# Kernel optimization log

Measured on AMD Instinct MI355X. Metric: run time of the kernel, lower is better.

Reference implementation:

```python
import jax, jax.numpy as jnp
import numpy as np

D, H, FF, E, K, B, S = 1024, 16, 4096, 8, 2, 2, 2048
EPS = 1e-5


def _layernorm(x, g, b):
    mu = x.mean(-1, keepdims=True)
    var = x.var(-1, keepdims=True)
    return (x - mu) * jax.lax.rsqrt(var + EPS) * g + b


def setup_inputs() -> dict:
    key = jax.random.key(0)
    ks = jax.random.split(key, 16)
    s = 0.02
    return {
        "x": jax.random.normal(ks[0], (B, S, D), dtype=jnp.float32),
        "in_proj_w": jax.random.normal(ks[1], (3 * D, D), dtype=jnp.float32) * s,
        "in_proj_b": jnp.zeros((3 * D,), jnp.float32),
        "out_proj_w": jax.random.normal(ks[2], (D, D), dtype=jnp.float32) * s,
        "out_proj_b": jnp.zeros((D,), jnp.float32),
        "ln1_g": jnp.ones((D,), jnp.float32),
        "ln1_b": jnp.zeros((D,), jnp.float32),
        "ln2_g": jnp.ones((D,), jnp.float32),
        "ln2_b": jnp.zeros((D,), jnp.float32),
        "gate_w": jax.random.normal(ks[3], (E, D), dtype=jnp.float32) * s,
        "gate_b": jnp.zeros((E,), jnp.float32),
        "w1": jax.random.normal(ks[4], (E, FF, D), dtype=jnp.float32) * s,
        "b1": jnp.zeros((E, FF), jnp.float32),
        "w2": jax.random.normal(ks[5], (E, D, FF), dtype=jnp.float32) * s,
        "b2": jnp.zeros((E, D), jnp.float32),
    }


def reference(x, in_proj_w, in_proj_b, out_proj_w, out_proj_b,
              ln1_g, ln1_b, ln2_g, ln2_b,
              gate_w, gate_b, w1, b1, w2, b2):
    b, s, d = x.shape
    hd = d // H
    # --- self-attention (pre-LN), dropout = identity (eval) ---
    normed = _layernorm(x, ln1_g, ln1_b)
    qkv = normed @ in_proj_w.T + in_proj_b            # [b,s,3d]
    q, k, v = jnp.split(qkv, 3, axis=-1)
    q = q.reshape(b, s, H, hd).transpose(0, 2, 1, 3)  # [b,h,s,hd]
    k = k.reshape(b, s, H, hd).transpose(0, 2, 1, 3)
    v = v.reshape(b, s, H, hd).transpose(0, 2, 1, 3)
    scores = jnp.einsum('bhqe,bhke->bhqk', q, k) / np.sqrt(hd)
    attn = jax.nn.softmax(scores, axis=-1)
    o = jnp.einsum('bhqk,bhke->bhqe', attn, v)
    o = o.transpose(0, 2, 1, 3).reshape(b, s, d)
    attn_out = o @ out_proj_w.T + out_proj_b
    x = x + attn_out
    present_kv = (normed, normed)
    # --- MoE FFN ---
    n2 = _layernorm(x, ln2_g, ln2_b)
    xf = n2.reshape(-1, d)                             # [T,d]
    T = xf.shape[0]
    logits = xf @ gate_w.T + gate_b                    # [T,E]
    probs = jax.nn.softmax(logits, axis=-1)
    top_v, top_i = jax.lax.top_k(probs, K)             # [T,K]
    top_v = top_v / top_v.sum(-1, keepdims=True)
    # combine weights per (token, expert); topk indices are unique per token
    cw = jnp.zeros((T, E), probs.dtype).at[jnp.arange(T)[:, None], top_i].add(top_v)
    # dense all-experts FFN (mathematically identical to masked gather/scatter)
    h = jnp.einsum('td,efd->etf', xf, w1) + b1[:, None, :]   # [E,T,FF]
    h = jax.nn.gelu(h, approximate=False)
    eo = jnp.einsum('etf,edf->etd', h, w2) + b2[:, None, :]  # [E,T,d]
    moe_out = jnp.einsum('te,etd->td', cw, eo)               # [T,d]
    out = x + moe_out.reshape(b, s, d)
    # --- load balance loss (Switch) ---
    top1 = jnp.argmax(probs, axis=-1)
    f = jnp.mean(jax.nn.one_hot(top1, E, dtype=probs.dtype), axis=0)
    P = probs.mean(axis=0)
    load_loss = 0.01 * E * jnp.sum(f * P)
    return out, load_loss, probs.reshape(b, s, E), present_kv[0]
```

## Files before the change

kernel.cpp:

```cpp
#include <hip/hip_runtime.h>
#include <math.h>

#define D_ 1024
#define H_ 16
#define HD_ 64
#define FF_ 4096
#define E_ 8
#define B_ 2
#define S_ 2048
#define T_ 4096
#define MAXROWS 9216
#define MAXTILES 72

typedef unsigned short u16;
typedef __attribute__((ext_vector_type(4))) float f32x4;
typedef __attribute__((ext_vector_type(8))) __bf16 bf16x8;
typedef __attribute__((ext_vector_type(8))) _Float16 f16x8;
typedef __attribute__((ext_vector_type(4))) unsigned short u16x4;

__device__ __forceinline__ u16 f2bf(float f){
  union { float f; unsigned u; } v; v.f = f;
  unsigned r = v.u + 0x7fffu + ((v.u >> 16) & 1u);
  return (u16)(r >> 16);
}
__device__ __forceinline__ float bf2f(u16 h){
  union { unsigned u; float f; } v; v.u = ((unsigned)h) << 16;
  return v.f;
}
__device__ __forceinline__ void glds16(const void* g, void* l){
  __builtin_amdgcn_global_load_lds((const __attribute__((address_space(1))) void*)g,
                                   (__attribute__((address_space(3))) void*)l, 16, 0, 0);
}
__device__ __forceinline__ bf16x8 ld8(const u16* p){
  return *reinterpret_cast<const bf16x8*>(p);
}
__device__ __forceinline__ f16x8 ldH8(const _Float16* p){
  return *reinterpret_cast<const f16x8*>(p);
}
__device__ __forceinline__ f32x4 mfma16(bf16x8 a, bf16x8 b, f32x4 c){
  return __builtin_amdgcn_mfma_f32_16x16x32_bf16(a, b, c, 0, 0, 0);
}
__device__ __forceinline__ f32x4 mfmaH(f16x8 a, f16x8 b, f32x4 c){
  return __builtin_amdgcn_mfma_f32_16x16x32_f16(a, b, c, 0, 0, 0);
}
__device__ __forceinline__ unsigned pk16(float a, float b){
  auto pk = __builtin_amdgcn_cvt_pkrtz(a, b);
  return __builtin_bit_cast(unsigned, pk);
}

__global__ void __launch_bounds__(256) split_hl_f16_kernel(const float* __restrict__ in,
    _Float16* __restrict__ hi, _Float16* __restrict__ lo, int n4){
  int i = blockIdx.x*blockDim.x + threadIdx.x;
  if (i >= n4) return;
  float4 v = reinterpret_cast<const float4*>(in)[i];
  float vv[4] = {v.x, v.y, v.z, v.w};
  u16x4 h, l;
  #pragma unroll
  for (int j=0;j<4;j++){
    const _Float16 hh = (_Float16)vv[j];
    const _Float16 ll = (_Float16)(vv[j] - (float)hh);
    h[j] = __builtin_bit_cast(u16, hh);
    l[j] = __builtin_bit_cast(u16, ll);
  }
  reinterpret_cast<u16x4*>(hi)[i] = h;
  reinterpret_cast<u16x4*>(lo)[i] = l;
}

__global__ void __launch_bounds__(256) cvt_bf_kernel(const float* __restrict__ in, u16* __restrict__ out, int n4){
  int i = blockIdx.x*blockDim.x + threadIdx.x;
  if (i >= n4) return;
  float4 v = reinterpret_cast<const float4*>(in)[i];
  u16x4 o;
  o[0]=f2bf(v.x); o[1]=f2bf(v.y); o[2]=f2bf(v.z); o[3]=f2bf(v.w);
  reinterpret_cast<u16x4*>(out)[i] = o;
}

__global__ void __launch_bounds__(256) cvt_f16_kernel(const float* __restrict__ in, _Float16* __restrict__ out, int n4){
  int i = blockIdx.x*blockDim.x + threadIdx.x;
  if (i >= n4) return;
  float4 v = reinterpret_cast<const float4*>(in)[i];
  union { unsigned w[2]; u16x4 u; } o;
  o.w[0] = pk16(v.x, v.y);
  o.w[1] = pk16(v.z, v.w);
  reinterpret_cast<u16x4*>(out)[i] = o.u;
}

template<int OUTMODE, int GATE>
__global__ void __launch_bounds__(256) ln_kernel(const float* __restrict__ x, const float* __restrict__ g,
    const float* __restrict__ bta, float* __restrict__ outf, u16* __restrict__ nout,
    const float* __restrict__ gw, const float* __restrict__ gb,
    float* __restrict__ probs_out, int* __restrict__ top_i, float* __restrict__ cw_w)
{
  const int t = blockIdx.x, tid = threadIdx.x;
  __shared__ float rs[4], rq[4];
  __shared__ float sp[4][E_];
  const float4 v = reinterpret_cast<const float4*>(x + (size_t)t*D_)[tid];
  float s  = v.x+v.y+v.z+v.w;
  float s2 = v.x*v.x+v.y*v.y+v.z*v.z+v.w*v.w;
  #pragma unroll
  for (int o=32;o;o>>=1){ s += __shfl_xor(s,o); s2 += __shfl_xor(s2,o); }
  const int wid=tid>>6, lane=tid&63;
  if (lane==0){ rs[wid]=s; rq[wid]=s2; }
  __syncthreads();
  s  = rs[0]+rs[1]+rs[2]+rs[3];
  s2 = rq[0]+rq[1]+rq[2]+rq[3];
  const float mu  = s*(1.0f/D_);
  const float var = s2*(1.0f/D_) - mu*mu;
  const float inv = rsqrtf(var + 1e-5f);
  const float4 gv = reinterpret_cast<const float4*>(g)[tid];
  const float4 bv = reinterpret_cast<const float4*>(bta)[tid];
  float oo[4];
  oo[0] = (v.x-mu)*inv*gv.x + bv.x;
  oo[1] = (v.y-mu)*inv*gv.y + bv.y;
  oo[2] = (v.z-mu)*inv*gv.z + bv.z;
  oo[3] = (v.w-mu)*inv*gv.w + bv.w;
  const size_t base = (size_t)t*D_ + tid*4;
  if (outf){ outf[base]=oo[0]; outf[base+1]=oo[1]; outf[base+2]=oo[2]; outf[base+3]=oo[3]; }
  if (OUTMODE==1){
    union { unsigned w[2]; u16x4 u; } hv;
    hv.w[0] = pk16(oo[0], oo[1]);
    hv.w[1] = pk16(oo[2], oo[3]);
    reinterpret_cast<u16x4*>(nout)[base>>2] = hv.u;
  } else {
    u16x4 hv;
    hv[0]=f2bf(oo[0]); hv[1]=f2bf(oo[1]); hv[2]=f2bf(oo[2]); hv[3]=f2bf(oo[3]);
    reinterpret_cast<u16x4*>(nout)[base>>2] = hv;
  }
  if (GATE){
    float part[E_];
    #pragma unroll
    for (int e=0;e<E_;e++){
      const float4 wv = reinterpret_cast<const float4*>(gw + (size_t)e*D_)[tid];
      part[e] = oo[0]*wv.x + oo[1]*wv.y + oo[2]*wv.z + oo[3]*wv.w;
    }
    #pragma unroll
    for (int e=0;e<E_;e++){
      #pragma unroll
      for (int o=32;o;o>>=1) part[e] += __shfl_xor(part[e], o);
    }
    if (lane==0){
      #pragma unroll
      for (int e=0;e<E_;e++) sp[wid][e] = part[e];
    }
    __syncthreads();
    if (tid==0){
      float lg[E_], mx=-3e38f;
      #pragma unroll
      for (int e=0;e<E_;e++){
        lg[e] = sp[0][e]+sp[1][e]+sp[2][e]+sp[3][e] + gb[e];
        mx = fmaxf(mx, lg[e]);
      }
      float ex[E_], sm=0.f;
      #pragma unroll
      for (int e=0;e<E_;e++){ ex[e]=__expf(lg[e]-mx); sm+=ex[e]; }
      float p[E_];
      #pragma unroll
      for (int e=0;e<E_;e++){ p[e]=ex[e]/sm; probs_out[(size_t)t*E_+e]=p[e]; }
      int i0=0; float l0=lg[0];
      #pragma unroll
      for (int e=1;e<E_;e++) if (lg[e]>l0){ l0=lg[e]; i0=e; }
      int i1=-1; float l1=-3e38f;
      #pragma unroll
      for (int e=0;e<E_;e++) if (e!=i0 && lg[e]>l1){ l1=lg[e]; i1=e; }
      top_i[2*t]=i0; top_i[2*t+1]=i1;
      const float v0=p[i0], v1=p[i1];
      const float swt=v0+v1;
      cw_w[2*t]=v0/swt; cw_w[2*t+1]=v1/swt;
    }
  }
}

__global__ void __launch_bounds__(256) qkv_kernel(
    const _Float16* __restrict__ A, const _Float16* __restrict__ Bw,
    const float* __restrict__ bias,
    _Float16* __restrict__ qf, _Float16* __restrict__ kf, _Float16* __restrict__ vtf)
{
  __shared__ __align__(16) _Float16 Ash[2][128*32], Bsh[2][128*32];
  const int bid = blockIdx.x, nwg = gridDim.x;
  const int fid = (bid & 7)*(nwg>>3) + (bid>>3);
  const int nt = fid % 24, mt = fid / 24;
  const int tid=threadIdx.x, wid=tid>>6, lane=tid&63;
  const int wr=wid>>1, wc=wid&1;
  const int r16=lane&15, g4=lane>>4;
  const _Float16* Ag = A  + (size_t)mt*128*D_;
  const _Float16* Bg = Bw + (size_t)nt*128*D_;
  const int srow = wid*16 + (lane>>2);
  const int scol = (((lane&3) ^ ((lane>>3)&3)))*8;
  const int sl   = (g4 ^ ((r16>>1)&3))*8;
  f32x4 acc[4][4] = {};
#define QSTAGE(bi, k0) do { \
    _Pragma("unroll") \
    for (int p=0;p<2;p++){ \
      const int r  = p*64 + srow; \
      const int lo = (p*64 + wid*16)*32; \
      glds16(Ag + (size_t)r*D_ + (k0) + scol, &Ash[bi][lo]); \
      glds16(Bg + (size_t)r*D_ + (k0) + scol, &Bsh[bi][lo]); \
    } \
  } while(0)
  QSTAGE(0, 0);
  int cur = 0;
  for (int t=0; t<D_/32; ++t){
    if (t+1 < D_/32){
      QSTAGE(cur^1, (t+1)*32);
      asm volatile("s_waitcnt vmcnt(4)" ::: "memory");
    } else {
      asm volatile("s_waitcnt vmcnt(0)" ::: "memory");
    }
    __syncthreads();
    f16x8 af[4], bfr[4];
    #pragma unroll
    for (int m=0;m<4;m++) af[m]=ldH8(&Ash[cur][(wr*64+m*16+r16)*32 + sl]);
    #pragma unroll
    for (int n=0;n<4;n++) bfr[n]=ldH8(&Bsh[cur][(wc*64+n*16+r16)*32 + sl]);
    #pragma unroll
    for (int m=0;m<4;m++){
      #pragma unroll
      for (int n=0;n<4;n++) acc[m][n] = mfmaH(af[m], bfr[n], acc[m][n]);
    }
    __syncthreads();
    cur ^= 1;
  }
#undef QSTAGE
  #pragma unroll
  for (int m=0;m<4;m++){
    #pragma unroll
    for (int n=0;n<4;n++){
      #pragma unroll
      for (int r=0;r<4;r++){
        const int grow = mt*128 + wr*64 + m*16 + g4*4 + r;
        const int gcol = nt*128 + wc*64 + n*16 + r16;
        const float val = acc[m][n][r] + bias[gcol];
        const int which = gcol>>10, rem = gcol&1023;
        const int hh = rem>>6, ee = rem&63;
        const int bb = grow>>11, ss = grow&2047;
        if (which==0){
          qf[((size_t)(bb*H_+hh)*S_ + ss)*HD_ + ee] = (_Float16)(val * 0.18033688f);
        } else if (which==1){
          kf[((size_t)(bb*H_+hh)*S_ + ss)*HD_ + ee] = (_Float16)val;
        } else {
          const int p32 = 2*(ss & 12) + (ss & 3) + 4*((ss >> 4) & 1);
          const size_t idx = (((size_t)(bb*H_+hh)*(S_/32) + (ss>>5))*HD_ + ee)*32 + p32;
          vtf[idx] = (_Float16)val;
        }
      }
    }
  }
}

__global__ void __launch_bounds__(256) gemm3_kernel(
    const _Float16* __restrict__ A, int lda,
    const _Float16* __restrict__ Bh, const _Float16* __restrict__ Bl, int Kdim,
    const float* __restrict__ bias,
    const float* __restrict__ resid, float* __restrict__ x1out)
{
  __shared__ __align__(16) _Float16 Ash[2][128*32], Bsh[2][128*32], Bsl[2][128*32];
  const int bid = blockIdx.x, nwg = gridDim.x;
  const int fid = (bid & 7)*(nwg>>3) + (bid>>3);
  const int nt = fid & 7, mt = fid >> 3;
  const int tid=threadIdx.x, wid=tid>>6, lane=tid&63;
  const int wr=wid>>1, wc=wid&1;
  const int r16=lane&15, g4=lane>>4;
  const _Float16* Ag  = A  + (size_t)mt*128*lda;
  const _Float16* Bgh = Bh + (size_t)nt*128*Kdim;
  const _Float16* Bgl = Bl + (size_t)nt*128*Kdim;
  const int srow = wid*16 + (lane>>2);
  const int scol = (((lane&3) ^ ((lane>>3)&3)))*8;
  const int sl   = (g4 ^ ((r16>>1)&3))*8;
  f32x4 acc[4][4] = {};
#define G3STAGE(bi, k0) do { \
    _Pragma("unroll") \
    for (int p=0;p<2;p++){ \
      const int r  = p*64 + srow; \
      const int lo = (p*64 + wid*16)*32; \
      glds16(Ag  + (size_t)r*lda  + (k0) + scol, &Ash[bi][lo]); \
      glds16(Bgh + (size_t)r*Kdim + (k0) + scol, &Bsh[bi][lo]); \
      glds16(Bgl + (size_t)r*Kdim + (k0) + scol, &Bsl[bi][lo]); \
    } \
  } while(0)
  G3STAGE(0, 0);
  int cur = 0;
  const int NK = Kdim/32;
  for (int t=0; t<NK; ++t){
    if (t+1 < NK){
      G3STAGE(cur^1, (t+1)*32);
      asm volatile("s_waitcnt vmcnt(6)" ::: "memory");
    } else {
      asm volatile("s_waitcnt vmcnt(0)" ::: "memory");
    }
    __syncthreads();
    f16x8 af[4], bfh[4], bfl[4];
    #pragma unroll
    for (int m=0;m<4;m++){
      const int row = wr*64 + m*16 + r16;
      af[m] = ldH8(&Ash[cur][row*32 + sl]);
    }
    #pragma unroll
    for (int n=0;n<4;n++){
      const int row = wc*64 + n*16 + r16;
      bfh[n] = ldH8(&Bsh[cur][row*32 + sl]);
      bfl[n] = ldH8(&Bsl[cur][row*32 + sl]);
    }
    #pragma unroll
    for (int m=0;m<4;m++){
      #pragma unroll
      for (int n=0;n<4;n++){
        acc[m][n] = mfmaH(af[m], bfl[n], acc[m][n]);
        acc[m][n] = mfmaH(af[m], bfh[n], acc[m][n]);
      }
    }
    __syncthreads();
    cur ^= 1;
  }
#undef G3STAGE
  #pragma unroll
  for (int m=0;m<4;m++){
    #pragma unroll
    for (int n=0;n<4;n++){
      #pragma unroll
      for (int r=0;r<4;r++){
        const int grow = mt*128 + wr*64 + m*16 + g4*4 + r;
        const int gcol = nt*128 + wc*64 + n*16 + r16;
        const float val = acc[m][n][r] + bias[gcol];
        const size_t idx = (size_t)grow*D_ + gcol;
        x1out[idx] = val + resid[idx];
      }
    }
  }
}

__global__ void __launch_bounds__(256) attn9_kernel(
    const _Float16* __restrict__ Qf, const _Float16* __restrict__ Kf,
    const _Float16* __restrict__ Vtf,
    _Float16* __restrict__ Of)
{
  __shared__ __align__(16) _Float16 Kb[2][4096];
  __shared__ __align__(16) _Float16 Vb[2][4096];
  const int bid = blockIdx.x;
  const int wg = (bid & 7) * 128 + (bid >> 3);
  const int bh = wg >> 5, qc = wg & 31;
  const int tid=threadIdx.x, wid=tid>>6, lane=tid&63;
  const int r16=lane&15, g4=lane>>4;
  const int q0 = qc*64 + wid*16;
  const _Float16* Qp = Qf  + (size_t)bh*S_*HD_ + (size_t)(q0+r16)*HD_ + g4*8;
  const _Float16* Kbase = Kf  + (size_t)bh*S_*HD_;
  const _Float16* Vbase = Vtf + (size_t)bh*HD_*S_;
  const f16x8 qf0 = ldH8(Qp);
  const f16x8 qf1 = ldH8(Qp+32);
  f32x4 of[4] = {};
  float m_run = -3e38f, lr = 0.f;

  const int kOff = (wid*8 + (lane>>3))*HD_ + (((lane&7) ^ ((lane>>3)&7)))*8;
  const int vOff = wid*512 + lane*8;
  const int sk0 = (g4 ^ (r16&7))*8;
  const int sk1 = ((g4+4) ^ (r16&7))*8;

#define STAGE(bi, tt) do { \
    glds16(Kbase + (size_t)(tt)*64*HD_ + kOff,          (void*)&Kb[bi][wid*512]); \
    glds16(Kbase + (size_t)(tt)*64*HD_ + 32*HD_ + kOff, (void*)&Kb[bi][2048 + wid*512]); \
    glds16(Vbase + (size_t)(tt)*4096 + vOff,            (void*)&Vb[bi][wid*512]); \
    glds16(Vbase + (size_t)(tt)*4096 + 2048 + vOff,     (void*)&Vb[bi][2048 + wid*512]); \
  } while(0)

#define ATT_HALF(Kh_, Vh_) do { \
    const f16x8 k0v = ldH8((Kh_) + r16*64 + sk0); \
    const f16x8 k1v = ldH8((Kh_) + r16*64 + sk1); \
    const f16x8 k2v = ldH8((Kh_) + (16+r16)*64 + sk0); \
    const f16x8 k3v = ldH8((Kh_) + (16+r16)*64 + sk1); \
    f32x4 sA={}, sB={}; \
    __builtin_amdgcn_s_setprio(1); \
    sA = mfmaH(k0v, qf0, sA); sA = mfmaH(k1v, qf1, sA); \
    sB = mfmaH(k2v, qf0, sB); sB = mfmaH(k3v, qf1, sB); \
    __builtin_amdgcn_s_setprio(0); \
    const float t0=sA[0], t1=sA[1], t2=sA[2], t3=sA[3]; \
    const float t4=sB[0], t5=sB[1], t6=sB[2], t7=sB[3]; \
    const float lmx = fmaxf(fmaxf(fmaxf(t0,t1),fmaxf(t2,t3)), \
                            fmaxf(fmaxf(t4,t5),fmaxf(t6,t7))); \
    if (!__all(lmx <= m_run + 4.0f)) { \
      float mx = fmaxf(lmx, __shfl_xor(lmx,16)); \
      mx = fmaxf(mx, __shfl_xor(mx,32)); \
      const float mn = fmaxf(m_run, mx); \
      const float alp = __builtin_amdgcn_exp2f(m_run - mn); \
      m_run = mn; \
      lr *= alp; \
      const float ao0=__shfl(alp,4*g4), ao1=__shfl(alp,4*g4+1); \
      const float ao2=__shfl(alp,4*g4+2), ao3=__shfl(alp,4*g4+3); \
      _Pragma("unroll") \
      for (int c=0;c<4;c++){ of[c][0]*=ao0; of[c][1]*=ao1; of[c][2]*=ao2; of[c][3]*=ao3; } \
    } \
    const float msh = m_run - 9.0f; \
    const float p0=__builtin_amdgcn_exp2f(t0-msh), p1=__builtin_amdgcn_exp2f(t1-msh); \
    const float p2=__builtin_amdgcn_exp2f(t2-msh), p3=__builtin_amdgcn_exp2f(t3-msh); \
    const float p4=__builtin_amdgcn_exp2f(t4-msh), p5=__builtin_amdgcn_exp2f(t5-msh); \
    const float p6=__builtin_amdgcn_exp2f(t6-msh), p7=__builtin_amdgcn_exp2f(t7-msh); \
    lr += ((p0+p1)+(p2+p3)) + ((p4+p5)+(p6+p7)); \
    union { unsigned w[4]; f16x8 v; } pu; \
    pu.w[0]=pk16(p0,p1); pu.w[1]=pk16(p2,p3); \
    pu.w[2]=pk16(p4,p5); pu.w[3]=pk16(p6,p7); \
    const f16x8 v0v = ldH8((Vh_) + (r16)*32 + g4*8); \
    const f16x8 v1v = ldH8((Vh_) + (16+r16)*32 + g4*8); \
    const f16x8 v2v = ldH8((Vh_) + (32+r16)*32 + g4*8); \
    const f16x8 v3v = ldH8((Vh_) + (48+r16)*32 + g4*8); \
    __builtin_amdgcn_s_setprio(1); \
    of[0] = mfmaH(pu.v, v0v, of[0]); of[1] = mfmaH(pu.v, v1v, of[1]); \
    of[2] = mfmaH(pu.v, v2v, of[2]); of[3] = mfmaH(pu.v, v3v, of[3]); \
    __builtin_amdgcn_s_setprio(0); \
  } while(0)

  STAGE(0, 0);
  int cur = 0;

  for (int t=0; t<32; ++t){
    if (t < 31){
      STAGE(cur^1, t+1);
      asm volatile("s_waitcnt vmcnt(4)" ::: "memory");
    } else {
      asm volatile("s_waitcnt vmcnt(0)" ::: "memory");
    }
    __syncthreads();
    ATT_HALF(&Kb[cur][0],    &Vb[cur][0]);
    ATT_HALF(&Kb[cur][2048], &Vb[cur][2048]);
    __syncthreads();
    cur ^= 1;
  }
#undef ATT_HALF
#undef STAGE

  lr += __shfl_xor(lr,16);
  lr += __shfl_xor(lr,32);
  float li[4];
  #pragma unroll
  for (int r=0;r<4;r++) li[r] = 1.0f / __shfl(lr, 4*g4+r);
  const int bb = bh>>4, hh = bh&15;
  #pragma unroll
  for (int c=0;c<4;c++){
    #pragma unroll
    for (int r=0;r<4;r++){
      const float val = of[c][r] * li[r];
      const int qq = q0 + 4*g4 + r;
      const size_t idx = ((size_t)(bb*S_+qq))*D_ + hh*HD_ + c*16 + r16;
      Of[idx] = (_Float16)val;
    }
  }
}

__global__ void __launch_bounds__(512) scan_kernel(const int* __restrict__ top_i,
    int* __restrict__ goff, int* __restrict__ tile_expert,
    int* __restrict__ assign_token, int* __restrict__ pos_of)
{
  __shared__ int cnt[E_];
  __shared__ int off[E_+1];
  const int tid=threadIdx.x;
  if (tid<E_) cnt[tid]=0;
  __syncthreads();
  for (int t=tid;t<T_;t+=512){
    atomicAdd(&cnt[top_i[2*t]],1);
    atomicAdd(&cnt[top_i[2*t+1]],1);
  }
  __syncthreads();
  if (tid==0){
    off[0]=0;
    for (int e=0;e<E_;e++) off[e+1]=off[e]+((cnt[e]+127)&~127);
    for (int i=0;i<=E_;i++) goff[i]=off[i];
  }
  __syncthreads();
  if (tid<MAXTILES){
    const int r=tid*128; int e=-1;
    for (int j=0;j<E_;j++) if (r>=off[j] && r<off[j+1]) e=j;
    tile_expert[tid]=e;
  }
  const int lane=tid&63;
  const int e=tid>>6;
  int base=off[e];
  for (int c=0;c<T_/64;c++){
    const int t=c*64+lane;
    const int a0=top_i[2*t], a1=top_i[2*t+1];
    const bool f=(a0==e)||(a1==e);
    const unsigned long long m=__ballot(f);
    if (f){
      const int pos = base + (int)__popcll(m & ((1ull<<lane)-1ull));
      assign_token[pos]=t;
      pos_of[2*t + (a0==e?0:1)] = pos;
    }
    base += (int)__popcll(m);
  }
  for (int r=base+lane; r<off[e+1]; r+=64) assign_token[r]=-1;
  __syncthreads();
  for (int r=off[E_]+tid; r<MAXROWS; r+=512) assign_token[r]=-1;
}

template<int MODE>
__global__ void __launch_bounds__(256, 4) gemm_grp_kernel(
    const u16* __restrict__ A, int lda,
    const u16* __restrict__ Bbase, int Kdim, int Nsz, int NT,
    const float* __restrict__ bias,
    const int* __restrict__ tile_expert,
    const int* __restrict__ atok,
    u16* __restrict__ outp)
{
  const int bid = blockIdx.x, nwg = gridDim.x;
  const int fid = (bid & 7)*(nwg>>3) + (bid>>3);
  const int nt = fid % NT, mt = fid / NT;
  const int e = tile_expert[mt];
  if (e<0) return;
  __shared__ __align__(16) u16 Ash[2][128*32], Bsh[2][128*32];
  const int tid=threadIdx.x, wid=tid>>6, lane=tid&63;
  const int wr=wid>>1, wc=wid&1;
  const int r16=lane&15, g4=lane>>4;
  const float* bp = bias + (size_t)e*Nsz;
  const int srow = wid*16 + (lane>>2);
  const int scol = (((lane&3) ^ ((lane>>3)&3)))*8;
  const int sl   = (g4 ^ ((r16>>1)&3))*8;
  const u16* Bg = Bbase + (size_t)e*Nsz*Kdim + (size_t)nt*128*Kdim;
  size_t arow0, arow1;
  if (MODE==2){
    int t0 = atok[mt*128 + srow];      if (t0 < 0) t0 = 0;
    int t1 = atok[mt*128 + 64 + srow]; if (t1 < 0) t1 = 0;
    arow0 = (size_t)t0*lda;
    arow1 = (size_t)t1*lda;
  } else {
    arow0 = (size_t)(mt*128 + srow)*lda;
    arow1 = (size_t)(mt*128 + 64 + srow)*lda;
  }
  f32x4 acc[4][4] = {};
#define GSTAGE(bi, k0) do { \
    glds16(A + arow0 + (k0) + scol, &Ash[bi][(wid*16)*32]); \
    glds16(A + arow1 + (k0) + scol, &Ash[bi][(64 + wid*16)*32]); \
    glds16(Bg + (size_t)(srow)*Kdim      + (k0) + scol, &Bsh[bi][(wid*16)*32]); \
    glds16(Bg + (size_t)(64+srow)*Kdim   + (k0) + scol, &Bsh[bi][(64 + wid*16)*32]); \
  } while(0)
  GSTAGE(0, 0);
  int cur = 0;
  const int NK = Kdim/32;
  for (int t=0; t<NK; ++t){
    if (t+1 < NK){
      GSTAGE(cur^1, (t+1)*32);
      asm volatile("s_waitcnt vmcnt(4)" ::: "memory");
    } else {
      asm volatile("s_waitcnt vmcnt(0)" ::: "memory");
    }
    __syncthreads();
    bf16x8 af[4], bfr[4];
    #pragma unroll
    for (int m=0;m<4;m++) af[m]=ld8(&Ash[cur][(wr*64+m*16+r16)*32 + sl]);
    #pragma unroll
    for (int n=0;n<4;n++) bfr[n]=ld8(&Bsh[cur][(wc*64+n*16+r16)*32 + sl]);
    #pragma unroll
    for (int m=0;m<4;m++){
      #pragma unroll
      for (int n=0;n<4;n++) acc[m][n] = mfma16(af[m], bfr[n], acc[m][n]);
    }
    __syncthreads();
    cur ^= 1;
  }
#undef GSTAGE
  #pragma unroll
  for (int m=0;m<4;m++){
    #pragma unroll
    for (int n=0;n<4;n++){
      #pragma unroll
      for (int r=0;r<4;r++){
        const int grow = mt*128 + wr*64 + m*16 + g4*4 + r;
        const int gcol = nt*128 + wc*64 + n*16 + r16;
        float val = acc[m][n][r] + bp[gcol];
        if (MODE==2){
          const float z = val*(1.0f + 0.044715f*val*val)*2.3021622f;
          val = val / (1.0f + __builtin_amdgcn_exp2f(-z));
        }
        outp[(size_t)grow*Nsz + gcol] = f2bf(val);
      }
    }
  }
}

__global__ void __launch_bounds__(256) combine_kernel(const float* __restrict__ x1,
    const u16* __restrict__ eo, const int* __restrict__ pos_of, const float* __restrict__ cw_w,
    float* __restrict__ out0)
{
  const int t=blockIdx.x, tid=threadIdx.x;
  const int r0=pos_of[2*t], r1=pos_of[2*t+1];
  const float w0=cw_w[2*t], w1=cw_w[2*t+1];
  const u16x4 e0 = reinterpret_cast<const u16x4*>(eo + (size_t)r0*D_)[tid];
  const u16x4 e1 = reinterpret_cast<const u16x4*>(eo + (size_t)r1*D_)[tid];
  const float4 xv = reinterpret_cast<const float4*>(x1 + (size_t)t*D_)[tid];
  float4 o;
  o.x = xv.x + w0*bf2f(e0[0]) + w1*bf2f(e1[0]);
  o.y = xv.y + w0*bf2f(e0[1]) + w1*bf2f(e1[1]);
  o.z = xv.z + w0*bf2f(e0[2]) + w1*bf2f(e1[2]);
  o.w = xv.w + w0*bf2f(e0[3]) + w1*bf2f(e1[3]);
  reinterpret_cast<float4*>(out0 + (size_t)t*D_)[tid] = o;
}

__global__ void __launch_bounds__(256) loss_kernel(const float* __restrict__ probs,
    const int* __restrict__ top_i, float* __restrict__ loss_out)
{
  const int tid=threadIdx.x;
  float f[E_]={0,0,0,0,0,0,0,0}, P[E_]={0,0,0,0,0,0,0,0};
  for (int t=tid;t<T_;t+=256){
    const float* pr = probs + (size_t)t*E_;
    const int a0 = top_i[2*t];
    #pragma unroll
    for (int e=0;e<E_;e++){
      P[e] += pr[e];
      f[e] += (a0==e) ? 1.0f : 0.0f;
    }
  }
  #pragma unroll
  for (int e=0;e<E_;e++){
    #pragma unroll
    for (int o=32;o;o>>=1){ f[e]+=__shfl_xor(f[e],o); P[e]+=__shfl_xor(P[e],o); }
  }
  __shared__ float sf[4][E_], sP[4][E_];
  const int wid=tid>>6, lane=tid&63;
  if (lane==0){
    #pragma unroll
    for (int e=0;e<E_;e++){ sf[wid][e]=f[e]; sP[wid][e]=P[e]; }
  }
  __syncthreads();
  if (tid==0){
    float loss=0.f;
    #pragma unroll
    for (int e=0;e<E_;e++){
      const float fe=sf[0][e]+sf[1][e]+sf[2][e]+sf[3][e];
      const float Pe=sP[0][e]+sP[1][e]+sP[2][e]+sP[3][e];
      loss += (fe/(float)T_)*(Pe/(float)T_);
    }
    loss_out[0] = 0.01f*(float)E_*loss;
  }
}

static inline size_t alup(size_t x){ return (x+255)&~(size_t)255; }

extern "C" void kernel_launch(void* const* d_in, const int* in_sizes, int n_in,
                              void* d_out, int out_size, void* d_ws, size_t ws_size,
                              hipStream_t stream) {
  (void)in_sizes; (void)n_in; (void)out_size; (void)ws_size;
  const float* x    = (const float*)d_in[0];
  const float* ipw  = (const float*)d_in[1];
  const float* ipb  = (const float*)d_in[2];
  const float* opw  = (const float*)d_in[3];
  const float* opb  = (const float*)d_in[4];
  const float* ln1g = (const float*)d_in[5];
  const float* ln1b = (const float*)d_in[6];
  const float* ln2g = (const float*)d_in[7];
  const float* ln2b = (const float*)d_in[8];
  const float* gw   = (const float*)d_in[9];
  const float* gb   = (const float*)d_in[10];
  const float* w1   = (const float*)d_in[11];
  const float* b1   = (const float*)d_in[12];
  const float* w2   = (const float*)d_in[13];
  const float* b2   = (const float*)d_in[14];

  float* out0       = (float*)d_out;
  float* loss_out   = out0 + (size_t)T_*D_;
  float* probs_out  = loss_out + 1;
  float* normed_out = probs_out + (size_t)T_*E_;

  char* p = (char*)d_ws;
  auto take = [&](size_t bytes)->void*{ void* r = (void*)p; p += alup(bytes); return r; };

  _Float16* wipf  = (_Float16*)take((size_t)3*D_*D_*2);
  _Float16* wophf = (_Float16*)take((size_t)D_*D_*2);
  _Float16* woplf = (_Float16*)take((size_t)D_*D_*2);
  u16* w1b   = (u16*)take((size_t)E_*FF_*D_*2);
  u16* w2b   = (u16*)take((size_t)E_*D_*FF_*2);
  _Float16* nf16 = (_Float16*)take((size_t)T_*D_*2);
  _Float16* qf  = (_Float16*)take((size_t)T_*D_*2);
  _Float16* kf  = (_Float16*)take((size_t)T_*D_*2);
  _Float16* vtf = (_Float16*)take((size_t)T_*D_*2);
  _Float16* of16 = (_Float16*)take((size_t)T_*D_*2);
  float* x1  = (float*)take((size_t)T_*D_*4);
  u16* n2b   = (u16*)take((size_t)T_*D_*2);
  u16* hbuf  = (u16*)take((size_t)MAXROWS*FF_*2);
  u16* eo    = (u16*)take((size_t)MAXROWS*D_*2);
  int* top_i = (int*)take((size_t)T_*2*4);
  float* cww = (float*)take((size_t)T_*2*4);
  int* posof = (int*)take((size_t)T_*2*4);
  int* goff  = (int*)take((size_t)(E_+1)*4);
  int* texp  = (int*)take((size_t)MAXTILES*4);
  int* atok  = (int*)take((size_t)MAXROWS*4);

  cvt_f16_kernel<<<(3*D_*D_/4+255)/256, 256, 0, stream>>>(ipw, wipf, 3*D_*D_/4);
  split_hl_f16_kernel<<<(D_*D_/4+255)/256, 256, 0, stream>>>(opw, wophf, woplf, D_*D_/4);
  cvt_bf_kernel<<<(E_*FF_*D_/4+255)/256, 256, 0, stream>>>(w1, w1b, E_*FF_*D_/4);
  cvt_bf_kernel<<<(E_*D_*FF_/4+255)/256, 256, 0, stream>>>(w2, w2b, E_*D_*FF_/4);

  ln_kernel<1,0><<<T_, 256, 0, stream>>>(x, ln1g, ln1b, normed_out, (u16*)nf16,
                                         nullptr, nullptr, nullptr, nullptr, nullptr);

  qkv_kernel<<<dim3(24*(T_/128)), 256, 0, stream>>>(nf16, wipf, ipb, qf, kf, vtf);

  attn9_kernel<<<B_*H_*(S_/64), 256, 0, stream>>>(qf, kf, vtf, of16);

  gemm3_kernel<<<dim3(8*(T_/128)), 256, 0, stream>>>(
      of16, D_, wophf, woplf, D_, opb, x, x1);

  ln_kernel<2,1><<<T_, 256, 0, stream>>>(x1, ln2g, ln2b, nullptr, n2b,
                                         gw, gb, probs_out, top_i, cww);

  scan_kernel<<<1, 512, 0, stream>>>(top_i, goff, texp, atok, posof);

  gemm_grp_kernel<2><<<dim3((FF_/128)*MAXTILES), 256, 0, stream>>>(n2b, D_, w1b, D_, FF_, FF_/128, b1, texp, atok, hbuf);
  gemm_grp_kernel<3><<<dim3((D_/128)*MAXTILES), 256, 0, stream>>>(hbuf, FF_, w2b, FF_, D_, D_/128, b2, texp, nullptr, eo);

  combine_kernel<<<T_, 256, 0, stream>>>(x1, eo, posof, cww, out0);
  loss_kernel<<<1, 256, 0, stream>>>(probs_out, top_i, loss_out);
}
```

Before: 518.5 us.

## Widen attention blocks to 512 threads and fuse small kernels

The attention kernel now uses 8 waves per block covering 128 queries. Each block still stages one 64-key K/V tile per step, now sharing it across twice as many query rows, which halves K/V global traffic per query. The two bf16 weight conversion launches become one combined launch, and the load-balance loss is folded into the single-block scan kernel to remove a launch. The larger blocks may lower occupancy, and the scan kernel now does extra serial work.

```diff
diff --git a/kernel.cpp b/kernel.cpp
--- a/kernel.cpp
+++ b/kernel.cpp
@@ -66,13 +66,17 @@
   reinterpret_cast<u16x4*>(lo)[i] = l;
 }
 
-__global__ void __launch_bounds__(256) cvt_bf_kernel(const float* __restrict__ in, u16* __restrict__ out, int n4){
+__global__ void __launch_bounds__(256) cvt_bf2_kernel(
+    const float* __restrict__ in1, u16* __restrict__ out1,
+    const float* __restrict__ in2, u16* __restrict__ out2, int n4each){
   int i = blockIdx.x*blockDim.x + threadIdx.x;
-  if (i >= n4) return;
-  float4 v = reinterpret_cast<const float4*>(in)[i];
+  const float* in; u16* out; int j;
+  if (i < n4each){ in = in1; out = out1; j = i; }
+  else           { in = in2; out = out2; j = i - n4each; }
+  float4 v = reinterpret_cast<const float4*>(in)[j];
   u16x4 o;
   o[0]=f2bf(v.x); o[1]=f2bf(v.y); o[2]=f2bf(v.z); o[3]=f2bf(v.w);
-  reinterpret_cast<u16x4*>(out)[i] = o;
+  reinterpret_cast<u16x4*>(out)[j] = o;
 }
 
 __global__ void __launch_bounds__(256) cvt_f16_kernel(const float* __restrict__ in, _Float16* __restrict__ out, int n4){
@@ -328,7 +332,7 @@
   }
 }
 
-__global__ void __launch_bounds__(256) attn9_kernel(
+__global__ void __launch_bounds__(512, 2) attn10_kernel(
     const _Float16* __restrict__ Qf, const _Float16* __restrict__ Kf,
     const _Float16* __restrict__ Vtf,
     _Float16* __restrict__ Of)
@@ -336,11 +340,11 @@
   __shared__ __align__(16) _Float16 Kb[2][4096];
   __shared__ __align__(16) _Float16 Vb[2][4096];
   const int bid = blockIdx.x;
-  const int wg = (bid & 7) * 128 + (bid >> 3);
-  const int bh = wg >> 5, qc = wg & 31;
+  const int wg = (bid & 7) * 64 + (bid >> 3);
+  const int bh = wg >> 4, qc = wg & 15;
   const int tid=threadIdx.x, wid=tid>>6, lane=tid&63;
   const int r16=lane&15, g4=lane>>4;
-  const int q0 = qc*64 + wid*16;
+  const int q0 = qc*128 + wid*16;
   const _Float16* Qp = Qf  + (size_t)bh*S_*HD_ + (size_t)(q0+r16)*HD_ + g4*8;
   const _Float16* Kbase = Kf  + (size_t)bh*S_*HD_;
   const _Float16* Vbase = Vtf + (size_t)bh*HD_*S_;
@@ -355,10 +359,8 @@
   const int sk1 = ((g4+4) ^ (r16&7))*8;
 
 #define STAGE(bi, tt) do { \
-    glds16(Kbase + (size_t)(tt)*64*HD_ + kOff,          (void*)&Kb[bi][wid*512]); \
-    glds16(Kbase + (size_t)(tt)*64*HD_ + 32*HD_ + kOff, (void*)&Kb[bi][2048 + wid*512]); \
-    glds16(Vbase + (size_t)(tt)*4096 + vOff,            (void*)&Vb[bi][wid*512]); \
-    glds16(Vbase + (size_t)(tt)*4096 + 2048 + vOff,     (void*)&Vb[bi][2048 + wid*512]); \
+    glds16(Kbase + (size_t)(tt)*64*HD_ + kOff, (void*)&Kb[bi][wid*512]); \
+    glds16(Vbase + (size_t)(tt)*4096   + vOff, (void*)&Vb[bi][wid*512]); \
   } while(0)
 
 #define ATT_HALF(Kh_, Vh_) do { \
@@ -412,7 +414,7 @@
   for (int t=0; t<32; ++t){
     if (t < 31){
       STAGE(cur^1, t+1);
-      asm volatile("s_waitcnt vmcnt(4)" ::: "memory");
+      asm volatile("s_waitcnt vmcnt(2)" ::: "memory");
     } else {
       asm volatile("s_waitcnt vmcnt(0)" ::: "memory");
     }
@@ -445,10 +447,12 @@
 
 __global__ void __launch_bounds__(512) scan_kernel(const int* __restrict__ top_i,
     int* __restrict__ goff, int* __restrict__ tile_expert,
-    int* __restrict__ assign_token, int* __restrict__ pos_of)
+    int* __restrict__ assign_token, int* __restrict__ pos_of,
+    const float* __restrict__ probs, float* __restrict__ loss_out)
 {
   __shared__ int cnt[E_];
   __shared__ int off[E_+1];
+  __shared__ float sf[8][E_], sP[8][E_];
   const int tid=threadIdx.x;
   if (tid<E_) cnt[tid]=0;
   __syncthreads();
@@ -486,6 +490,38 @@
   for (int r=base+lane; r<off[e+1]; r+=64) assign_token[r]=-1;
   __syncthreads();
   for (int r=off[E_]+tid; r<MAXROWS; r+=512) assign_token[r]=-1;
+  float fc[E_]={0,0,0,0,0,0,0,0}, Ps[E_]={0,0,0,0,0,0,0,0};
+  for (int t=tid;t<T_;t+=512){
+    const float* pr = probs + (size_t)t*E_;
+    const int a0 = top_i[2*t];
+    #pragma unroll
+    for (int k=0;k<E_;k++){
+      Ps[k] += pr[k];
+      fc[k] += (a0==k) ? 1.0f : 0.0f;
+    }
+  }
+  #pragma unroll
+  for (int k=0;k<E_;k++){
+    #pragma unroll
+    for (int o=32;o;o>>=1){ fc[k]+=__shfl_xor(fc[k],o); Ps[k]+=__shfl_xor(Ps[k],o); }
+  }
+  const int wid8 = tid>>6;
+  if (lane==0){
+    #pragma unroll
+    for (int k=0;k<E_;k++){ sf[wid8][k]=fc[k]; sP[wid8][k]=Ps[k]; }
+  }
+  __syncthreads();
+  if (tid==0){
+    float loss=0.f;
+    #pragma unroll
+    for (int k=0;k<E_;k++){
+      float fe=0.f, Pe=0.f;
+      #pragma unroll
+      for (int w=0;w<8;w++){ fe+=sf[w][k]; Pe+=sP[w][k]; }
+      loss += (fe/(float)T_)*(Pe/(float)T_);
+    }
+    loss_out[0] = 0.01f*(float)E_*loss;
+  }
 }
 
 template<int MODE>
@@ -590,44 +626,6 @@
   reinterpret_cast<float4*>(out0 + (size_t)t*D_)[tid] = o;
 }
 
-__global__ void __launch_bounds__(256) loss_kernel(const float* __restrict__ probs,
-    const int* __restrict__ top_i, float* __restrict__ loss_out)
-{
-  const int tid=threadIdx.x;
-  float f[E_]={0,0,0,0,0,0,0,0}, P[E_]={0,0,0,0,0,0,0,0};
-  for (int t=tid;t<T_;t+=256){
-    const float* pr = probs + (size_t)t*E_;
-    const int a0 = top_i[2*t];
-    #pragma unroll
-    for (int e=0;e<E_;e++){
-      P[e] += pr[e];
-      f[e] += (a0==e) ? 1.0f : 0.0f;
-    }
-  }
-  #pragma unroll
-  for (int e=0;e<E_;e++){
-    #pragma unroll
-    for (int o=32;o;o>>=1){ f[e]+=__shfl_xor(f[e],o); P[e]+=__shfl_xor(P[e],o); }
-  }
-  __shared__ float sf[4][E_], sP[4][E_];
-  const int wid=tid>>6, lane=tid&63;
-  if (lane==0){
-    #pragma unroll
-    for (int e=0;e<E_;e++){ sf[wid][e]=f[e]; sP[wid][e]=P[e]; }
-  }
-  __syncthreads();
-  if (tid==0){
-    float loss=0.f;
-    #pragma unroll
-    for (int e=0;e<E_;e++){
-      const float fe=sf[0][e]+sf[1][e]+sf[2][e]+sf[3][e];
-      const float Pe=sP[0][e]+sP[1][e]+sP[2][e]+sP[3][e];
-      loss += (fe/(float)T_)*(Pe/(float)T_);
-    }
-    loss_out[0] = 0.01f*(float)E_*loss;
-  }
-}
-
 static inline size_t alup(size_t x){ return (x+255)&~(size_t)255; }
 
 extern "C" void kernel_launch(void* const* d_in, const int* in_sizes, int n_in,
@@ -681,15 +679,14 @@
 
   cvt_f16_kernel<<<(3*D_*D_/4+255)/256, 256, 0, stream>>>(ipw, wipf, 3*D_*D_/4);
   split_hl_f16_kernel<<<(D_*D_/4+255)/256, 256, 0, stream>>>(opw, wophf, woplf, D_*D_/4);
-  cvt_bf_kernel<<<(E_*FF_*D_/4+255)/256, 256, 0, stream>>>(w1, w1b, E_*FF_*D_/4);
-  cvt_bf_kernel<<<(E_*D_*FF_/4+255)/256, 256, 0, stream>>>(w2, w2b, E_*D_*FF_/4);
+  cvt_bf2_kernel<<<(2*(E_*FF_*D_/4)+255)/256, 256, 0, stream>>>(w1, w1b, w2, w2b, E_*FF_*D_/4);
 
   ln_kernel<1,0><<<T_, 256, 0, stream>>>(x, ln1g, ln1b, normed_out, (u16*)nf16,
                                          nullptr, nullptr, nullptr, nullptr, nullptr);
 
   qkv_kernel<<<dim3(24*(T_/128)), 256, 0, stream>>>(nf16, wipf, ipb, qf, kf, vtf);
 
-  attn9_kernel<<<B_*H_*(S_/64), 256, 0, stream>>>(qf, kf, vtf, of16);
+  attn10_kernel<<<B_*H_*(S_/128), 512, 0, stream>>>(qf, kf, vtf, of16);
 
   gemm3_kernel<<<dim3(8*(T_/128)), 256, 0, stream>>>(
       of16, D_, wophf, woplf, D_, opb, x, x1);
@@ -697,11 +694,10 @@
   ln_kernel<2,1><<<T_, 256, 0, stream>>>(x1, ln2g, ln2b, nullptr, n2b,
                                          gw, gb, probs_out, top_i, cww);
 
-  scan_kernel<<<1, 512, 0, stream>>>(top_i, goff, texp, atok, posof);
+  scan_kernel<<<1, 512, 0, stream>>>(top_i, goff, texp, atok, posof, probs_out, loss_out);
 
   gemm_grp_kernel<2><<<dim3((FF_/128)*MAXTILES), 256, 0, stream>>>(n2b, D_, w1b, D_, FF_, FF_/128, b1, texp, atok, hbuf);
   gemm_grp_kernel<3><<<dim3((D_/128)*MAXTILES), 256, 0, stream>>>(hbuf, FF_, w2b, FF_, D_, D_/128, b2, texp, nullptr, eo);
 
   combine_kernel<<<T_, 256, 0, stream>>>(x1, eo, posof, cww, out0);
-  loss_kernel<<<1, 256, 0, stream>>>(probs_out, top_i, loss_out);
-}
+}
```

New measurement: 499.7 us. 1.04x faster.
